# Kernel optimization log

Hardware: AMD Instinct MI355X
Metric: run time of the kernel (lower is better)

Reference implementation:

```python
import jax, jax.numpy as jnp
import numpy as np

K = 1024
H = 16

def setup_inputs() -> dict:
    key = jax.random.key(0)
    ks = jax.random.split(key, 6)
    s = 1.0 / np.sqrt(K)
    return {
        "x": jax.random.normal(ks[0], (2, 2048, K), dtype=jnp.float32),
        "Wq": jax.random.uniform(ks[1], (K, K), jnp.float32, -s, s),
        "Wk": jax.random.uniform(ks[2], (K, K), jnp.float32, -s, s),
        "Wv": jax.random.uniform(ks[3], (K, K), jnp.float32, -s, s),
        "Wu": jax.random.uniform(ks[4], (K, K), jnp.float32, -s, s),
        "bu": jax.random.uniform(ks[5], (K,), jnp.float32, -s, s),
    }

def reference(x, Wq, Wk, Wv, Wu, bu):
    b, t, k = x.shape
    hd = k // H  # head dim = 64
    scale = jnp.asarray(k, x.dtype) ** 0.25  # Bloem-style: scale q and k each by k^(1/4)
    # nn.Linear(bias=False): y = x @ W.T
    q = (jnp.einsum('btk,ok->bto', x, Wq) / scale).reshape(b, t, H, hd)
    kk = (jnp.einsum('btk,ok->bto', x, Wk) / scale).reshape(b, t, H, hd)
    v = jnp.einsum('btk,ok->bto', x, Wv).reshape(b, t, H, hd)
    dot = jnp.einsum('bthd,bshd->bhts', q, kk)  # [b,h,t,t]
    att = jax.nn.softmax(dot, axis=-1)
    out = jnp.einsum('bhts,bshd->bthd', att, v).reshape(b, t, k)
    return jnp.einsum('btk,ok->bto', out, Wu) + bu
```

## Files before the change

kernel.cpp:

```cpp
#include <hip/hip_runtime.h>

typedef __bf16 bf16;
typedef bf16  bf16x8 __attribute__((ext_vector_type(8)));
typedef bf16  bf16x4 __attribute__((ext_vector_type(4)));
typedef float f32x4  __attribute__((ext_vector_type(4)));

#define MFMA16(a, b, c) __builtin_amdgcn_mfma_f32_16x16x32_bf16((a), (b), (c), 0, 0, 0)
#define AS1 __attribute__((address_space(1)))
#define AS3 __attribute__((address_space(3)))

__device__ __forceinline__ void gld_lds16(const bf16* g, bf16* l) {
    __builtin_amdgcn_global_load_lds((AS1 void*)(g), (AS3 void*)(l), 16, 0, 0);
}


__global__ __launch_bounds__(256) void cvt_all(const float* __restrict__ x,
                                               const float* __restrict__ Wq, const float* __restrict__ Wk,
                                               const float* __restrict__ Wv, const float* __restrict__ Wu,
                                               bf16* ox, bf16* oq, bf16* ok, bf16* ov, bf16* ou,
                                               float sq, float sk) {
    int bid = blockIdx.x;
    const float* src; bf16* dst; float sc; int base;
    if (bid < 4096) { src = x; dst = ox; sc = 1.0f; base = bid; }
    else {
        int w = (bid - 4096) >> 10; base = (bid - 4096) & 1023;
        switch (w) {
            case 0:  src = Wq; dst = oq; sc = sq;   break;
            case 1:  src = Wk; dst = ok; sc = sk;   break;
            case 2:  src = Wv; dst = ov; sc = 1.0f; break;
            default: src = Wu; dst = ou; sc = 1.0f; break;
        }
    }
    int idx = (base * 256 + threadIdx.x) * 4;
    float4 v = *(const float4*)(src + idx);
    bf16x4 o;
    o[0] = (bf16)(v.x * sc); o[1] = (bf16)(v.y * sc);
    o[2] = (bf16)(v.z * sc); o[3] = (bf16)(v.w * sc);
    *(bf16x4*)(dst + idx) = o;
}

__device__ __forceinline__ void gemm_core(const bf16* __restrict__ A, const bf16* __restrict__ B,
                                          int mBase, int nBase, bf16* As, bf16* Bs,
                                          f32x4 acc[4][4]) {
    const int tid = threadIdx.x;
    const int wave = tid >> 6, lane = tid & 63;
    const int g = lane >> 4, lr = lane & 15;
    const int wm = (wave & 1) << 6, wn = (wave >> 1) << 6;
    const int q = lane >> 2;
    const int cswz = ((lane & 3) ^ ((lane >> 3) & 3)) << 3;
    const int pcs  = (g ^ ((lr >> 1) & 3)) << 3;

    const int rb0 = wave << 4, rb1 = rb0 + 64;
    const bf16* a0 = A + (size_t)(mBase + rb0 + q) * 1024 + cswz;
    const bf16* a1 = A + (size_t)(mBase + rb1 + q) * 1024 + cswz;
    const bf16* b0 = B + (size_t)(nBase + rb0 + q) * 1024 + cswz;
    const bf16* b1 = B + (size_t)(nBase + rb1 + q) * 1024 + cswz;

    for (int k0 = 0; k0 < 1024; k0 += 32) {
        __syncthreads();
        gld_lds16(a0 + k0, As + rb0 * 32);
        gld_lds16(a1 + k0, As + rb1 * 32);
        gld_lds16(b0 + k0, Bs + rb0 * 32);
        gld_lds16(b1 + k0, Bs + rb1 * 32);
        __syncthreads();

        bf16x8 af[4], bfr[4];
#pragma unroll
        for (int i = 0; i < 4; i++)
            af[i] = *(const bf16x8*)&As[(wm + (i << 4) + lr) * 32 + pcs];
#pragma unroll
        for (int j = 0; j < 4; j++)
            bfr[j] = *(const bf16x8*)&Bs[(wn + (j << 4) + lr) * 32 + pcs];
#pragma unroll
        for (int i = 0; i < 4; i++)
#pragma unroll
            for (int j = 0; j < 4; j++)
                acc[i][j] = MFMA16(af[i], bfr[j], acc[i][j]);
    }
}

__global__ __launch_bounds__(256) void gemm_qkv(const bf16* __restrict__ X,
                                                const bf16* __restrict__ Wqk,
                                                const bf16* __restrict__ Wv,
                                                bf16* __restrict__ Qo, bf16* __restrict__ Ko,
                                                bf16* __restrict__ Vto) {
    __shared__ bf16 As[128 * 32];
    __shared__ bf16 Bs[128 * 32];
    const int tid = threadIdx.x;
    const int wave = tid >> 6, lane = tid & 63;
    const int g = lane >> 4, lr = lane & 15;
    const int wm = (wave & 1) << 6, wn = (wave >> 1) << 6;
    const int my = blockIdx.y;
    const bool qk = (my < 16);

    const bf16* Ap = qk ? Wqk : X;
    const bf16* Bp = qk ? X   : Wv;
    const int mBase = qk ? my * 128 : blockIdx.x * 128;
    const int nBase = qk ? blockIdx.x * 128 : (my - 16) * 128;

    f32x4 acc[4][4] = {};
    gemm_core(Ap, Bp, mBase, nBase, As, Bs, acc);

    if (qk) {
#pragma unroll
        for (int i = 0; i < 4; i++) {
            int m0 = mBase + wm + (i << 4) + (g << 2);
            bf16* dst = (m0 >> 10) ? Ko : Qo;
            int feat = m0 & 1023;
            int h = feat >> 6, d = feat & 63;
#pragma unroll
            for (int j = 0; j < 4; j++) {
                int t = nBase + wn + (j << 4) + lr;
                int b = t >> 11, tl = t & 2047;
                bf16x4 v;
#pragma unroll
                for (int r = 0; r < 4; r++) v[r] = (bf16)acc[i][j][r];
                *(bf16x4*)&dst[(((size_t)((b << 4) + h) * 2048 + tl) << 6) + d] = v;
            }
        }
    } else {
#pragma unroll
        for (int i = 0; i < 4; i++) {
            int t0 = mBase + wm + (i << 4) + (g << 2);
            int b = t0 >> 11, tl = t0 & 2047;
#pragma unroll
            for (int j = 0; j < 4; j++) {
                int o = nBase + wn + (j << 4) + lr;
                int h = o >> 6, d = o & 63;
                bf16x4 v;
#pragma unroll
                for (int r = 0; r < 4; r++) v[r] = (bf16)acc[i][j][r];
                *(bf16x4*)&Vto[((size_t)(((b << 4) + h) << 6) + d) * 2048 + tl] = v;
            }
        }
    }
}

__global__ __launch_bounds__(256) void gemm_out(const bf16* __restrict__ Wu, const bf16* __restrict__ A,
                                                const float* __restrict__ bias, float* __restrict__ out) {
    __shared__ bf16 As[128 * 32];
    __shared__ bf16 Bs[128 * 32];
    const int tid = threadIdx.x;
    const int wave = tid >> 6, lane = tid & 63;
    const int g = lane >> 4, lr = lane & 15;
    const int wm = (wave & 1) << 6, wn = (wave >> 1) << 6;
    const int mBase = blockIdx.y * 128, nBase = blockIdx.x * 128;

    f32x4 acc[4][4] = {};
    gemm_core(Wu, A, mBase, nBase, As, Bs, acc);

#pragma unroll
    for (int i = 0; i < 4; i++) {
        int o = mBase + wm + (i << 4) + (g << 2);
        float4 bv = *(const float4*)&bias[o];
#pragma unroll
        for (int j = 0; j < 4; j++) {
            int t = nBase + wn + (j << 4) + lr;
            float4 v;
            v.x = acc[i][j][0] + bv.x;
            v.y = acc[i][j][1] + bv.y;
            v.z = acc[i][j][2] + bv.z;
            v.w = acc[i][j][3] + bv.w;
            *(float4*)&out[((size_t)t << 10) + o] = v;
        }
    }
}

__global__ __launch_bounds__(256, 4) void attn(const bf16* __restrict__ Q, const bf16* __restrict__ Kt,
                                               const bf16* __restrict__ Vt, bf16* __restrict__ O) {
    __shared__ bf16 Ks[2][128][32];
    __shared__ bf16 Ps[64][128];
    float* Lbuf = (float*)&Ks[0][0][0];

    const int tid = threadIdx.x;
    const int wave = tid >> 6, lane = tid & 63;
    const int g = lane >> 4, lr = lane & 15;
    const int q = lane >> 2;
    const int cswz = ((lane & 3) ^ ((lane >> 3) & 3)) << 3;
    const int pcs  = (g ^ ((lr >> 1) & 3)) << 3;
    const int lr7  = lr & 7;
    const int thalf = wave >> 1, dhalf = wave & 1;

    const int bid = blockIdx.x;
    const int bh = ((bid & 7) << 2) | (bid >> 8);
    const int qBase = ((bid >> 3) & 31) << 6;

    const bf16* Qg = Q + ((size_t)bh * 2048 + qBase) * 64;
    const bf16* Kg = Kt + (size_t)bh * 2048 * 64;
    const bf16* Vg = Vt + (size_t)bh * 64 * 2048;

    bf16x8 qf[2][4];
#pragma unroll
    for (int ks = 0; ks < 2; ks++)
#pragma unroll
        for (int tt = 0; tt < 4; tt++)
            qf[ks][tt] = *(const bf16x8*)(Qg + ((tt << 4) + lr) * 64 + (ks << 5) + (g << 3));

    const int pw0 = ((((wave << 2) + (g >> 1))     ^ lr7) << 3) + ((g & 1) << 2);
    const int pw1 = ((((wave << 2) + 2 + (g >> 1)) ^ lr7) << 3) + ((g & 1) << 2);

    f32x4 oacc[2][2] = {};
    f32x4 lsumv[4] = {};

    for (int s0 = 0; s0 < 2048; s0 += 128) {
        __syncthreads();
#pragma unroll
        for (int i = 0; i < 4; i++) {
            int bi = (wave << 2) + i;
            int p = bi >> 3, rb = (bi & 7) << 4;
            gld_lds16(Kg + (size_t)(s0 + rb + q) * 64 + (p << 5) + cswz, &Ks[p][rb][0]);
        }
        __syncthreads();

#pragma unroll
        for (int isub = 0; isub < 2; isub++) {
            f32x4 sacc[4] = {};
#pragma unroll
            for (int ks = 0; ks < 2; ks++) {
                bf16x8 kf = *(const bf16x8*)&Ks[ks][(wave << 5) + (isub << 4) + lr][pcs];
#pragma unroll
                for (int tt = 0; tt < 4; tt++)
                    sacc[tt] = MFMA16(kf, qf[ks][tt], sacc[tt]);
            }
#pragma unroll
            for (int tt = 0; tt < 4; tt++) {
                f32x4 e;
                e[0] = __builtin_amdgcn_exp2f(sacc[tt][0]);
                e[1] = __builtin_amdgcn_exp2f(sacc[tt][1]);
                e[2] = __builtin_amdgcn_exp2f(sacc[tt][2]);
                e[3] = __builtin_amdgcn_exp2f(sacc[tt][3]);
                lsumv[tt] += e;
                bf16x4 pb;
                pb[0] = (bf16)e[0]; pb[1] = (bf16)e[1]; pb[2] = (bf16)e[2]; pb[3] = (bf16)e[3];
                *(bf16x4*)&Ps[(tt << 4) + lr][isub ? pw1 : pw0] = pb;
            }
        }
        __syncthreads();

#pragma unroll
        for (int ks2 = 0; ks2 < 4; ks2++) {
            bf16x8 vf[2], pf[2];
#pragma unroll
            for (int dd = 0; dd < 2; dd++)
                vf[dd] = *(const bf16x8*)(Vg + (size_t)((dhalf << 5) + (dd << 4) + lr) * 2048
                                          + s0 + (ks2 << 5) + (g << 3));
#pragma unroll
            for (int tt = 0; tt < 2; tt++)
                pf[tt] = *(const bf16x8*)&Ps[(thalf << 5) + (tt << 4) + lr]
                                            [(((ks2 << 2) + g) ^ lr7) << 3];
#pragma unroll
            for (int tt = 0; tt < 2; tt++)
#pragma unroll
                for (int dd = 0; dd < 2; dd++)
                    oacc[tt][dd] = MFMA16(pf[tt], vf[dd], oacc[tt][dd]);
        }
    }

    float lpart[4];
#pragma unroll
    for (int tt = 0; tt < 4; tt++) {
        lpart[tt] = (lsumv[tt][0] + lsumv[tt][1]) + (lsumv[tt][2] + lsumv[tt][3]);
        lpart[tt] += __shfl_xor(lpart[tt], 16, 64);
        lpart[tt] += __shfl_xor(lpart[tt], 32, 64);
    }
    __syncthreads();
    if (g == 0) {
#pragma unroll
        for (int tt = 0; tt < 4; tt++)
            Lbuf[(wave << 6) + (tt << 4) + lr] = lpart[tt];
    }
    __syncthreads();

    const int b = bh >> 4, h = bh & 15;
#pragma unroll
    for (int tt = 0; tt < 2; tt++) {
        float linv[4];
#pragma unroll
        for (int r = 0; r < 4; r++) {
            int t = (thalf << 5) + (tt << 4) + (g << 2) + r;
            linv[r] = 1.0f / (((Lbuf[t] + Lbuf[64 + t]) + (Lbuf[128 + t] + Lbuf[192 + t])));
        }
#pragma unroll
        for (int dd = 0; dd < 2; dd++)
#pragma unroll
            for (int r = 0; r < 4; r++) {
                int t = qBase + (thalf << 5) + (tt << 4) + (g << 2) + r;
                int col = (h << 6) + (dhalf << 5) + (dd << 4) + lr;
                O[(((size_t)(b * 2048 + t)) << 10) + col] = (bf16)(oacc[tt][dd][r] * linv[r]);
            }
    }
}

extern "C" void kernel_launch(void* const* d_in, const int* in_sizes, int n_in,
                              void* d_out, int out_size, void* d_ws, size_t ws_size,
                              hipStream_t stream) {
    const float* x  = (const float*)d_in[0];
    const float* Wq = (const float*)d_in[1];
    const float* Wk = (const float*)d_in[2];
    const float* Wv = (const float*)d_in[3];
    const float* Wu = (const float*)d_in[4];
    const float* bu = (const float*)d_in[5];
    float* out = (float*)d_out;

    char* ws = (char*)d_ws;
    bf16* xbf  = (bf16*)(ws);
    bf16* wqbf = (bf16*)(ws + ((size_t)8  << 20));
    bf16* wkbf = (bf16*)(ws + ((size_t)10 << 20));
    bf16* wvbf = (bf16*)(ws + ((size_t)12 << 20));
    bf16* wubf = (bf16*)(ws + ((size_t)14 << 20));
    bf16* Qb   = (bf16*)(ws + ((size_t)16 << 20));
    bf16* Kb   = (bf16*)(ws + ((size_t)24 << 20));
    bf16* Vtb  = (bf16*)(ws + ((size_t)32 << 20));
    bf16* attnO = xbf;

    const float iscale_k = 0.17677669529663687f;
    const float iscale_q = 0.25503540109f;

    cvt_all<<<8192, 256, 0, stream>>>(x, Wq, Wk, Wv, Wu, xbf, wqbf, wkbf, wvbf, wubf,
                                      iscale_q, iscale_k);

    gemm_qkv<<<dim3(32, 24), 256, 0, stream>>>(xbf, wqbf, wvbf, Qb, Kb, Vtb);
    attn<<<dim3(1024), 256, 0, stream>>>(Qb, Kb, Vtb, attnO);
    gemm_out<<<dim3(32, 8), 256, 0, stream>>>(wubf, attnO, bu, out);
}
```

Baseline: 211.1 us.

## Split attention key range per wave and drop per-iteration block barriers

Each wave now owns its own 32-key slice of every 128-key tile. It reads K fragments straight from global memory instead of staging them in LDS, and keeps a private P buffer, so the two __syncthreads per iteration go away. Each wave accumulates a full 64x64 output partial, and the partials are reduced across the four waves through LDS in a tree at the end. The output is then staged and written as vectorized bf16x4 stores. In exchange, register pressure rises (oacc grows 4x and the occupancy launch bound is removed), global K loads are uncoalesced, and the epilogue adds extra LDS traffic and barriers.

```diff
diff --git a/kernel.cpp b/kernel.cpp
--- a/kernel.cpp
+++ b/kernel.cpp
@@ -12,7 +12,6 @@
 __device__ __forceinline__ void gld_lds16(const bf16* g, bf16* l) {
     __builtin_amdgcn_global_load_lds((AS1 void*)(g), (AS3 void*)(l), 16, 0, 0);
 }
-
 
 __global__ __launch_bounds__(256) void cvt_all(const float* __restrict__ x,
                                                const float* __restrict__ Wq, const float* __restrict__ Wk,
@@ -166,20 +165,16 @@
     }
 }
 
-__global__ __launch_bounds__(256, 4) void attn(const bf16* __restrict__ Q, const bf16* __restrict__ Kt,
-                                               const bf16* __restrict__ Vt, bf16* __restrict__ O) {
-    __shared__ bf16 Ks[2][128][32];
-    __shared__ bf16 Ps[64][128];
-    float* Lbuf = (float*)&Ks[0][0][0];
+__global__ __launch_bounds__(256) void attn(const bf16* __restrict__ Q, const bf16* __restrict__ Kt,
+                                            const bf16* __restrict__ Vt, bf16* __restrict__ O) {
+    __shared__ __align__(16) bf16 Ps[4][64][32];
+    __shared__ __align__(16) float Xtra[4352];
+    float* Obuf0 = (float*)&Ps[0][0][0];
 
     const int tid = threadIdx.x;
     const int wave = tid >> 6, lane = tid & 63;
     const int g = lane >> 4, lr = lane & 15;
-    const int q = lane >> 2;
-    const int cswz = ((lane & 3) ^ ((lane >> 3) & 3)) << 3;
-    const int pcs  = (g ^ ((lr >> 1) & 3)) << 3;
-    const int lr7  = lr & 7;
-    const int thalf = wave >> 1, dhalf = wave & 1;
+    const int lr3 = lr & 3;
 
     const int bid = blockIdx.x;
     const int bh = ((bid & 7) << 2) | (bid >> 8);
@@ -196,28 +191,23 @@
         for (int tt = 0; tt < 4; tt++)
             qf[ks][tt] = *(const bf16x8*)(Qg + ((tt << 4) + lr) * 64 + (ks << 5) + (g << 3));
 
-    const int pw0 = ((((wave << 2) + (g >> 1))     ^ lr7) << 3) + ((g & 1) << 2);
-    const int pw1 = ((((wave << 2) + 2 + (g >> 1)) ^ lr7) << 3) + ((g & 1) << 2);
-
-    f32x4 oacc[2][2] = {};
+    const int pwA = ((((g >> 1))     ^ lr3) << 3) + ((g & 1) << 2);
+    const int pwB = (((2 + (g >> 1)) ^ lr3) << 3) + ((g & 1) << 2);
+    const int prd = (g ^ lr3) << 3;
+
+    f32x4 oacc[4][4] = {};
     f32x4 lsumv[4] = {};
 
     for (int s0 = 0; s0 < 2048; s0 += 128) {
-        __syncthreads();
-#pragma unroll
-        for (int i = 0; i < 4; i++) {
-            int bi = (wave << 2) + i;
-            int p = bi >> 3, rb = (bi & 7) << 4;
-            gld_lds16(Kg + (size_t)(s0 + rb + q) * 64 + (p << 5) + cswz, &Ks[p][rb][0]);
-        }
-        __syncthreads();
+        const bf16* Kc = Kg + (size_t)(s0 + (wave << 5)) * 64;
+        const bf16* Vc = Vg + s0 + (wave << 5) + (g << 3);
 
 #pragma unroll
         for (int isub = 0; isub < 2; isub++) {
             f32x4 sacc[4] = {};
 #pragma unroll
             for (int ks = 0; ks < 2; ks++) {
-                bf16x8 kf = *(const bf16x8*)&Ks[ks][(wave << 5) + (isub << 4) + lr][pcs];
+                bf16x8 kf = *(const bf16x8*)(Kc + ((isub << 4) + lr) * 64 + (ks << 5) + (g << 3));
 #pragma unroll
                 for (int tt = 0; tt < 4; tt++)
                     sacc[tt] = MFMA16(kf, qf[ks][tt], sacc[tt]);
@@ -232,62 +222,95 @@
                 lsumv[tt] += e;
                 bf16x4 pb;
                 pb[0] = (bf16)e[0]; pb[1] = (bf16)e[1]; pb[2] = (bf16)e[2]; pb[3] = (bf16)e[3];
-                *(bf16x4*)&Ps[(tt << 4) + lr][isub ? pw1 : pw0] = pb;
-            }
-        }
-        __syncthreads();
-
-#pragma unroll
-        for (int ks2 = 0; ks2 < 4; ks2++) {
-            bf16x8 vf[2], pf[2];
-#pragma unroll
-            for (int dd = 0; dd < 2; dd++)
-                vf[dd] = *(const bf16x8*)(Vg + (size_t)((dhalf << 5) + (dd << 4) + lr) * 2048
-                                          + s0 + (ks2 << 5) + (g << 3));
-#pragma unroll
-            for (int tt = 0; tt < 2; tt++)
-                pf[tt] = *(const bf16x8*)&Ps[(thalf << 5) + (tt << 4) + lr]
-                                            [(((ks2 << 2) + g) ^ lr7) << 3];
-#pragma unroll
-            for (int tt = 0; tt < 2; tt++)
-#pragma unroll
-                for (int dd = 0; dd < 2; dd++)
-                    oacc[tt][dd] = MFMA16(pf[tt], vf[dd], oacc[tt][dd]);
-        }
-    }
-
-    float lpart[4];
+                *(bf16x4*)&Ps[wave][(tt << 4) + lr][isub ? pwB : pwA] = pb;
+            }
+        }
+
+        bf16x8 vf[4], pf[4];
+#pragma unroll
+        for (int jd = 0; jd < 4; jd++)
+            vf[jd] = *(const bf16x8*)(Vc + (size_t)((jd << 4) + lr) * 2048);
+#pragma unroll
+        for (int tt = 0; tt < 4; tt++)
+            pf[tt] = *(const bf16x8*)&Ps[wave][(tt << 4) + lr][prd];
+#pragma unroll
+        for (int tt = 0; tt < 4; tt++)
+#pragma unroll
+            for (int jd = 0; jd < 4; jd++)
+                oacc[tt][jd] = MFMA16(pf[tt], vf[jd], oacc[tt][jd]);
+    }
+
+    __syncthreads();
+    float lp[4];
 #pragma unroll
     for (int tt = 0; tt < 4; tt++) {
-        lpart[tt] = (lsumv[tt][0] + lsumv[tt][1]) + (lsumv[tt][2] + lsumv[tt][3]);
-        lpart[tt] += __shfl_xor(lpart[tt], 16, 64);
-        lpart[tt] += __shfl_xor(lpart[tt], 32, 64);
-    }
-    __syncthreads();
-    if (g == 0) {
-#pragma unroll
-        for (int tt = 0; tt < 4; tt++)
-            Lbuf[(wave << 6) + (tt << 4) + lr] = lpart[tt];
-    }
-    __syncthreads();
-
+        lp[tt] = (lsumv[tt][0] + lsumv[tt][1]) + (lsumv[tt][2] + lsumv[tt][3]);
+        lp[tt] += __shfl_xor(lp[tt], 16, 64);
+        lp[tt] += __shfl_xor(lp[tt], 32, 64);
+    }
+    if (lane < 16)
+#pragma unroll
+        for (int tt = 0; tt < 4; tt++)
+            Xtra[4096 + (wave << 6) + (tt << 4) + lr] = lp[tt];
+
+    if (wave >= 2) {
+        float* dst = (wave == 2) ? Obuf0 : Xtra;
+#pragma unroll
+        for (int tt = 0; tt < 4; tt++)
+#pragma unroll
+            for (int jd = 0; jd < 4; jd++)
+                *(f32x4*)&dst[((jd << 4) + lr) * 64 + (((((tt << 2) + g) ^ lr3)) << 2)] = oacc[tt][jd];
+    }
+    __syncthreads();
+    if (wave < 2) {
+        float* srcb = wave ? Xtra : Obuf0;
+#pragma unroll
+        for (int tt = 0; tt < 4; tt++)
+#pragma unroll
+            for (int jd = 0; jd < 4; jd++)
+                oacc[tt][jd] += *(f32x4*)&srcb[((jd << 4) + lr) * 64 + (((((tt << 2) + g) ^ lr3)) << 2)];
+    }
+    __syncthreads();
+    if (wave == 1) {
+#pragma unroll
+        for (int tt = 0; tt < 4; tt++)
+#pragma unroll
+            for (int jd = 0; jd < 4; jd++)
+                *(f32x4*)&Obuf0[((jd << 4) + lr) * 64 + (((((tt << 2) + g) ^ lr3)) << 2)] = oacc[tt][jd];
+    }
+    __syncthreads();
+    if (wave == 0) {
+#pragma unroll
+        for (int tt = 0; tt < 4; tt++) {
+#pragma unroll
+            for (int jd = 0; jd < 4; jd++)
+                oacc[tt][jd] += *(f32x4*)&Obuf0[((jd << 4) + lr) * 64 + (((((tt << 2) + g) ^ lr3)) << 2)];
+            f32x4 Ls = {};
+#pragma unroll
+            for (int w = 0; w < 4; w++)
+                Ls += *(const f32x4*)&Xtra[4096 + (w << 6) + (tt << 4) + (g << 2)];
+            f32x4 li;
+#pragma unroll
+            for (int r = 0; r < 4; r++) li[r] = 1.0f / Ls[r];
+#pragma unroll
+            for (int jd = 0; jd < 4; jd++) {
+                f32x4 v = oacc[tt][jd] * li;
+#pragma unroll
+                for (int r = 0; r < 4; r++)
+                    Xtra[((tt << 4) + (g << 2) + r) * 64 + (jd << 4) + lr] = v[r];
+            }
+        }
+    }
+    __syncthreads();
     const int b = bh >> 4, h = bh & 15;
 #pragma unroll
-    for (int tt = 0; tt < 2; tt++) {
-        float linv[4];
-#pragma unroll
-        for (int r = 0; r < 4; r++) {
-            int t = (thalf << 5) + (tt << 4) + (g << 2) + r;
-            linv[r] = 1.0f / (((Lbuf[t] + Lbuf[64 + t]) + (Lbuf[128 + t] + Lbuf[192 + t])));
-        }
-#pragma unroll
-        for (int dd = 0; dd < 2; dd++)
-#pragma unroll
-            for (int r = 0; r < 4; r++) {
-                int t = qBase + (thalf << 5) + (tt << 4) + (g << 2) + r;
-                int col = (h << 6) + (dhalf << 5) + (dd << 4) + lr;
-                O[(((size_t)(b * 2048 + t)) << 10) + col] = (bf16)(oacc[tt][dd][r] * linv[r]);
-            }
+    for (int i = 0; i < 4; i++) {
+        int tl = (wave << 4) + (i << 2) + g;
+        f32x4 v = *(const f32x4*)&Xtra[tl * 64 + (lr << 2)];
+        bf16x4 o4;
+#pragma unroll
+        for (int r = 0; r < 4; r++) o4[r] = (bf16)v[r];
+        *(bf16x4*)&O[(((size_t)(b * 2048 + qBase + tl)) << 10) + (h << 6) + (lr << 2)] = o4;
     }
 }
 
```

Result: slower. 224.6 us (+6.4%).
